# Kernel optimization log

Measured on AMD Instinct MI355X. Metric: run time of the kernel, lower is better.

Reference implementation:

```python
import jax, jax.numpy as jnp
import numpy as np

N_NODES = 100000
N_EDGES = 1600000
F_IN = 128
HID = 128
N_CLS = 40


def setup_inputs() -> dict:
    key = jax.random.key(0)
    ks = jax.random.split(key, 11)
    s = 0.05
    return {
        "X": jax.random.normal(ks[0], (N_NODES, F_IN), dtype=jnp.float32),
        "edge_index": jax.random.randint(ks[1], (2, N_EDGES), 0, N_NODES, dtype=jnp.int64),
        "enc_W": jax.random.normal(ks[2], (HID, F_IN), dtype=jnp.float32) * s,
        "enc_b": jax.random.normal(ks[3], (HID,), dtype=jnp.float32) * s,
        "W1": jax.random.normal(ks[4], (HID, HID), dtype=jnp.float32) * s,
        "b1": jax.random.normal(ks[5], (HID,), dtype=jnp.float32) * s,
        "W2": jax.random.normal(ks[6], (HID, HID), dtype=jnp.float32) * s,
        "b2": jax.random.normal(ks[7], (HID,), dtype=jnp.float32) * s,
        "dec_W": jax.random.normal(ks[8], (N_CLS, HID), dtype=jnp.float32) * s,
        "dec_b": jax.random.normal(ks[9], (N_CLS,), dtype=jnp.float32) * s,
    }


def reference(X, edge_index, enc_W, enc_b, W1, b1, W2, b2, dec_W, dec_b):
    N = X.shape[0]
    # --- add self-loops (PyG GCNConv default) ---
    loop = jnp.arange(N, dtype=edge_index.dtype)
    src = jnp.concatenate([edge_index[0], loop])  # message sources
    dst = jnp.concatenate([edge_index[1], loop])  # aggregation targets
    # --- symmetric normalization: D^{-1/2} A_hat D^{-1/2} ---
    deg = jax.ops.segment_sum(jnp.ones_like(src, dtype=X.dtype), dst, num_segments=N)
    dinv = jnp.where(deg > 0, jax.lax.rsqrt(deg), 0.0)
    norm = dinv[src] * dinv[dst]  # [E+N]

    def gcn_conv(x, W, b):
        h = x @ W.T                               # [N,H] linear transform
        msg = h[src] * norm[:, None]              # gather + scale  [E+N,H]
        agg = jax.ops.segment_sum(msg, dst, num_segments=N)  # scatter-sum
        return agg + b

    x = X @ enc_W.T + enc_b                       # encoder (single Linear)
    x = jax.nn.relu(gcn_conv(x, W1, b1))
    x = jax.nn.relu(gcn_conv(x, W2, b2))
    logits = x @ dec_W.T + dec_b                  # decoder (single Linear)
    return jax.nn.log_softmax(logits, axis=1)
```

## Files before the change

kernel.cpp:

```cpp
#include <hip/hip_runtime.h>
#include <hip/hip_bf16.h>
#include <cstdint>

typedef __bf16 bf16x8 __attribute__((ext_vector_type(8)));
typedef float  f32x4  __attribute__((ext_vector_type(4)));


__global__ __launch_bounds__(256) void bucket_hist_kernel(const int* __restrict__ dst,
                                                          int* __restrict__ bhist,
                                                          int E, int NBK, int shift) {
    __shared__ int lh[1024];
    int t = threadIdx.x;
    for (int i = t; i < 1024; i += 256) lh[i] = 0;
    __syncthreads();
#pragma unroll
    for (int v = 0; v < 4; ++v) {
        int idx = blockIdx.x * 4096 + (v * 256 + t) * 4;
        if (idx + 3 < E) {
            int4 d = *reinterpret_cast<const int4*>(&dst[idx]);
            atomicAdd(&lh[d.x >> shift], 1);
            atomicAdd(&lh[d.y >> shift], 1);
            atomicAdd(&lh[d.z >> shift], 1);
            atomicAdd(&lh[d.w >> shift], 1);
        } else {
            for (int k = 0; k < 4; ++k)
                if (idx + k < E) atomicAdd(&lh[dst[idx + k] >> shift], 1);
        }
    }
    __syncthreads();
    for (int i = t; i < NBK; i += 256)
        if (lh[i]) atomicAdd(&bhist[i], lh[i]);
}

__global__ __launch_bounds__(256) void bucket_scan_kernel(const int* __restrict__ bhist,
                                                          int* __restrict__ bbase,
                                                          int* __restrict__ bcur,
                                                          int NBK, int* __restrict__ offsetsN, int E) {
    int t = threadIdx.x;
    int v0[4]; int s = 0;
#pragma unroll
    for (int k = 0; k < 4; ++k) { int i = t * 4 + k; v0[k] = (i < NBK) ? bhist[i] : 0; s += v0[k]; }
    int lane = t & 63, w = t >> 6;
    int v = s;
#pragma unroll
    for (int o = 1; o < 64; o <<= 1) { int u = __shfl_up(v, o); if (lane >= o) v += u; }
    __shared__ int ws[4];
    if (lane == 63) ws[w] = v;
    __syncthreads();
    if (t == 0) { int r = 0; for (int i = 0; i < 4; ++i) { int x = ws[i]; ws[i] = r; r += x; } }
    __syncthreads();
    int run = ws[w] + (v - s);
#pragma unroll
    for (int k = 0; k < 4; ++k) {
        int i = t * 4 + k;
        if (i < NBK) { bbase[i] = run; bcur[i] = run; run += v0[k]; }
    }
    if (t == 255) bbase[NBK] = E;
    if (t == 0)   *offsetsN = E;
}

__global__ __launch_bounds__(256) void bin_edges_kernel(const int* __restrict__ src,
                                                        const int* __restrict__ dst,
                                                        int* __restrict__ bcur,
                                                        unsigned* __restrict__ binned,
                                                        int E, int NBK, int shift) {
    __shared__ int lh[1024];
    int t = threadIdx.x;
    int mask = (1 << shift) - 1;
    for (int i = t; i < 1024; i += 256) lh[i] = 0;
    __syncthreads();
    int sv[32], dv[32], rk[32];
#pragma unroll
    for (int v = 0; v < 8; ++v) {
        int idx = blockIdx.x * 8192 + (v * 256 + t) * 4;
        if (idx + 3 < E) {
            int4 s4 = *reinterpret_cast<const int4*>(&src[idx]);
            int4 d4 = *reinterpret_cast<const int4*>(&dst[idx]);
            sv[v * 4 + 0] = s4.x; sv[v * 4 + 1] = s4.y; sv[v * 4 + 2] = s4.z; sv[v * 4 + 3] = s4.w;
            dv[v * 4 + 0] = d4.x; dv[v * 4 + 1] = d4.y; dv[v * 4 + 2] = d4.z; dv[v * 4 + 3] = d4.w;
        } else {
            for (int k = 0; k < 4; ++k) {
                sv[v * 4 + k] = (idx + k < E) ? src[idx + k] : 0;
                dv[v * 4 + k] = (idx + k < E) ? dst[idx + k] : -1;
            }
        }
    }
#pragma unroll
    for (int k = 0; k < 32; ++k)
        if (dv[k] >= 0) rk[k] = atomicAdd(&lh[dv[k] >> shift], 1);
    __syncthreads();
    for (int i = t; i < NBK; i += 256) {
        int c = lh[i];
        lh[i] = c ? atomicAdd(&bcur[i], c) : 0;
    }
    __syncthreads();
#pragma unroll
    for (int k = 0; k < 32; ++k) {
        if (dv[k] >= 0) {
            int b = dv[k] >> shift;
            binned[lh[b] + rk[k]] = ((unsigned)sv[k] << shift) | (unsigned)(dv[k] & mask);
        }
    }
}

__global__ __launch_bounds__(256) void bucket_build_kernel(const unsigned* __restrict__ binned,
                                                           const int* __restrict__ bbase,
                                                           int* __restrict__ csr_src,
                                                           int* __restrict__ offsets,
                                                           float* __restrict__ dinv,
                                                           int N, int shift) {
    int b = blockIdx.x;
    int t = threadIdx.x;
    int node0 = b << shift;
    int npb = min(1 << shift, N - node0);
    int bb = bbase[b], be = bbase[b + 1];
    int mask = (1 << shift) - 1;
    __shared__ int ncnt[256], npre[256], ncur[256];
    ncnt[t] = 0;
    __syncthreads();
    for (int e = bb + t; e < be; e += 256) {
        unsigned p = binned[e];
        atomicAdd(&ncnt[p & mask], 1);
    }
    __syncthreads();
    int deg = (t < npb) ? ncnt[t] : 0;
    int v = deg;
    int lane = t & 63, w = t >> 6;
#pragma unroll
    for (int o = 1; o < 64; o <<= 1) { int u = __shfl_up(v, o); if (lane >= o) v += u; }
    __shared__ int ws[4];
    if (lane == 63) ws[w] = v;
    __syncthreads();
    if (t == 0) { int r = 0; for (int i = 0; i < 4; ++i) { int x = ws[i]; ws[i] = r; r += x; } }
    __syncthreads();
    int pre = bb + ws[w] + v - deg;
    npre[t] = pre; ncur[t] = 0;
    __syncthreads();
    for (int e = bb + t; e < be; e += 256) {
        unsigned p = binned[e];
        int l = p & mask;
        int r = atomicAdd(&ncur[l], 1);
        csr_src[npre[l] + r] = (int)(p >> shift);
    }
    if (t < npb) {
        int node = node0 + t;
        offsets[node] = pre;
        dinv[node] = rsqrtf((float)(deg + 1));
    }
}

__global__ __launch_bounds__(128) void prep_weights_kernel(const float* __restrict__ W1,
                                                           const float* __restrict__ encW,
                                                           const float* __restrict__ encb,
                                                           const float* __restrict__ W2,
                                                           const float* __restrict__ decW,
                                                           __hip_bfloat16* __restrict__ Wfb,
                                                           float* __restrict__ bff,
                                                           __hip_bfloat16* __restrict__ W2b,
                                                           __hip_bfloat16* __restrict__ decWb) {
    int i = blockIdx.x;
    int j = threadIdx.x;
    const float* w1r = W1 + (size_t)i * 128;
    float s0 = 0.f, s1 = 0.f, s2 = 0.f, s3 = 0.f;
    for (int k = 0; k < 128; k += 4) {
        s0 += w1r[k + 0] * encW[(size_t)(k + 0) * 128 + j];
        s1 += w1r[k + 1] * encW[(size_t)(k + 1) * 128 + j];
        s2 += w1r[k + 2] * encW[(size_t)(k + 2) * 128 + j];
        s3 += w1r[k + 3] * encW[(size_t)(k + 3) * 128 + j];
    }
    Wfb[(size_t)i * 128 + j] = __float2bfloat16((s0 + s1) + (s2 + s3));
    W2b[(size_t)i * 128 + j] = __float2bfloat16(W2[(size_t)i * 128 + j]);
    if (i < 48) decWb[(size_t)i * 128 + j] = __float2bfloat16(i < 40 ? decW[(size_t)i * 128 + j] : 0.f);
    float t = w1r[j] * encb[j];
#pragma unroll
    for (int o = 32; o; o >>= 1) t += __shfl_down(t, o);
    __shared__ float red[2];
    if ((j & 63) == 0) red[j >> 6] = t;
    __syncthreads();
    if (j == 0) bff[i] = red[0] + red[1];
}

__device__ inline bf16x8 cvt8(float4 lo, float4 hi) {
    union { unsigned short u[8]; bf16x8 v; } t;
    t.u[0] = __builtin_bit_cast(unsigned short, __float2bfloat16(lo.x));
    t.u[1] = __builtin_bit_cast(unsigned short, __float2bfloat16(lo.y));
    t.u[2] = __builtin_bit_cast(unsigned short, __float2bfloat16(lo.z));
    t.u[3] = __builtin_bit_cast(unsigned short, __float2bfloat16(lo.w));
    t.u[4] = __builtin_bit_cast(unsigned short, __float2bfloat16(hi.x));
    t.u[5] = __builtin_bit_cast(unsigned short, __float2bfloat16(hi.y));
    t.u[6] = __builtin_bit_cast(unsigned short, __float2bfloat16(hi.z));
    t.u[7] = __builtin_bit_cast(unsigned short, __float2bfloat16(hi.w));
    return t.v;
}

__global__ __launch_bounds__(256) void gemm_enc_kernel(const float* __restrict__ Ain,
                                                       const __hip_bfloat16* __restrict__ W,
                                                       const float* __restrict__ bias,
                                                       const float* __restrict__ dscale,
                                                       __hip_bfloat16* __restrict__ out, int M) {
    int lane = threadIdx.x & 63;
    int wave = threadIdx.x >> 6;
    int row0 = blockIdx.x * 128 + wave * 32;
    int kgrp = lane >> 4, cl = lane & 15;

    bf16x8 afrag[2][4];
#pragma unroll
    for (int rt = 0; rt < 2; ++rt) {
        int ar = row0 + rt * 16 + cl;
        if (ar >= M) ar = M - 1;
        const float* Ar = Ain + (size_t)ar * 128;
#pragma unroll
        for (int c = 0; c < 4; ++c) {
            const float4* q = reinterpret_cast<const float4*>(Ar + (4 * c + kgrp) * 8);
            afrag[rt][c] = cvt8(q[0], q[1]);
        }
    }

    f32x4 acc[2][8];
#pragma unroll
    for (int rt = 0; rt < 2; ++rt)
#pragma unroll
        for (int t = 0; t < 8; ++t) acc[rt][t] = {0.f, 0.f, 0.f, 0.f};

#pragma unroll
    for (int c = 0; c < 4; ++c) {
#pragma unroll
        for (int t = 0; t < 8; ++t) {
            bf16x8 bfrag = reinterpret_cast<const bf16x8*>(W + (size_t)(t * 16 + cl) * 128)[4 * c + kgrp];
            acc[0][t] = __builtin_amdgcn_mfma_f32_16x16x32_bf16(afrag[0][c], bfrag, acc[0][t], 0, 0, 0);
            acc[1][t] = __builtin_amdgcn_mfma_f32_16x16x32_bf16(afrag[1][c], bfrag, acc[1][t], 0, 0, 0);
        }
    }

#pragma unroll
    for (int rt = 0; rt < 2; ++rt) {
        int rbase = row0 + rt * 16 + kgrp * 4;
#pragma unroll
        for (int i = 0; i < 4; ++i) {
            int r = rbase + i;
            float sc = dscale[(r < M) ? r : (M - 1)];
#pragma unroll
            for (int t = 0; t < 8; ++t) {
                int col = t * 16 + cl;
                float v = (acc[rt][t][i] + bias[col]) * sc;
                unsigned int uv = __builtin_bit_cast(unsigned short, __float2bfloat16(v));
                unsigned int pv = (unsigned int)__shfl_xor((int)uv, 1);
                if (!(lane & 1) && r < M)
                    *reinterpret_cast<unsigned int*>(out + (size_t)r * 128 + col) = (uv & 0xffffu) | (pv << 16);
            }
        }
    }
}

template<int NPW>
__device__ __forceinline__ void agg_phase(const __hip_bfloat16* __restrict__ h,
                                          const int* __restrict__ csr,
                                          const int* __restrict__ offsets,
                                          const float* __restrict__ dinv,
                                          const float* __restrict__ bias,
                                          unsigned* lds, int tile0, int N) {
    int w = threadIdx.x >> 6, lane = threadIdx.x & 63;
    int bc = lane * 2;
    float2 bb = *reinterpret_cast<const float2*>(&bias[bc]);
    int base = tile0 + w * NPW;
    int oidx = base + (lane < NPW ? lane : NPW);
    if (oidx > N) oidx = N;
    int off = offsets[oidx];

    int j0a[NPW], dga[NPW], nda[NPW];
    unsigned qs[NPW];
#pragma unroll
    for (int i = 0; i < NPW; ++i) {
        int node = base + i;
        nda[i] = __builtin_amdgcn_readfirstlane((node < N) ? node : (N - 1));
        j0a[i] = __builtin_amdgcn_readfirstlane(__shfl(off, i));
        int j1 = __builtin_amdgcn_readfirstlane(__shfl(off, i + 1));
        dga[i] = j1 - j0a[i];
        qs[i] = *reinterpret_cast<const unsigned*>(&h[(size_t)nda[i] * 128 + bc]);
    }
    int sc[NPW][8];
#pragma unroll
    for (int i = 0; i < NPW; ++i)
#pragma unroll
        for (int k = 0; k < 8; ++k)
            sc[i][k] = csr[j0a[i] + k];
    unsigned qn[8];
#pragma unroll
    for (int k = 0; k < 8; ++k)
        qn[k] = *reinterpret_cast<const unsigned*>(&h[(size_t)sc[0][k] * 128 + bc]);

#pragma unroll
    for (int i = 0; i < NPW; ++i) {
        int j0 = j0a[i], dg = dga[i];
        int node = base + i;
        bool live = node < N;

        unsigned qc[8];
#pragma unroll
        for (int k = 0; k < 8; ++k) qc[k] = qn[k];
        if (i + 1 < NPW) {
#pragma unroll
            for (int k = 0; k < 8; ++k)
                qn[k] = *reinterpret_cast<const unsigned*>(&h[(size_t)sc[i + 1][k] * 128 + bc]);
        }

        float ax[8], ay[8];
        ax[0] = __builtin_bit_cast(float, qs[i] << 16);
        ay[0] = __builtin_bit_cast(float, qs[i] & 0xffff0000u);
#pragma unroll
        for (int k = 1; k < 8; ++k) { ax[k] = 0.f; ay[k] = 0.f; }

#pragma unroll
        for (int k = 0; k < 8; ++k) {
            unsigned q = (k < dg) ? qc[k] : 0u;
            ax[k] += __builtin_bit_cast(float, q << 16);
            ay[k] += __builtin_bit_cast(float, q & 0xffff0000u);
        }
        int nb = (dg + 7) >> 3;
        for (int b = 1; b < nb; ++b) {
            int jb = j0 + 8 * b;
            int s[8];
#pragma unroll
            for (int k = 0; k < 8; ++k) s[k] = csr[jb + k];
            unsigned q[8];
#pragma unroll
            for (int k = 0; k < 8; ++k)
                q[k] = *reinterpret_cast<const unsigned*>(&h[(size_t)s[k] * 128 + bc]);
            int rem = dg - 8 * b;
#pragma unroll
            for (int k = 0; k < 8; ++k) {
                unsigned qq = (k < rem) ? q[k] : 0u;
                ax[k] += __builtin_bit_cast(float, qq << 16);
                ay[k] += __builtin_bit_cast(float, qq & 0xffff0000u);
            }
        }

        float sx = ((ax[0] + ax[1]) + (ax[2] + ax[3])) + ((ax[4] + ax[5]) + (ax[6] + ax[7]));
        float sy = ((ay[0] + ay[1]) + (ay[2] + ay[3])) + ((ay[4] + ay[5]) + (ay[6] + ay[7]));
        float dd = dinv[nda[i]];
        float ox = fmaxf(dd * sx + bb.x, 0.f);
        float oy = fmaxf(dd * sy + bb.y, 0.f);
        unsigned ow = (unsigned)__builtin_bit_cast(unsigned short, __float2bfloat16(ox)) |
                      ((unsigned)__builtin_bit_cast(unsigned short, __float2bfloat16(oy)) << 16);
        if (!live) ow = 0u;
        int row = w * NPW + i;
        lds[row * 64 + (lane ^ ((row & 15) << 2))] = ow;
    }
}

__global__ __launch_bounds__(512, 8) void agg_gemm_kernel(const __hip_bfloat16* __restrict__ h,
                                                          const int* __restrict__ csr,
                                                          const int* __restrict__ offsets,
                                                          const float* __restrict__ dinv,
                                                          const float* __restrict__ bias,
                                                          const __hip_bfloat16* __restrict__ W,
                                                          __hip_bfloat16* __restrict__ out, int N) {
    __shared__ unsigned lds[32 * 64];
    int tile0 = blockIdx.x * 32;
    agg_phase<4>(h, csr, offsets, dinv, bias, lds, tile0, N);
    __syncthreads();

    int lane = threadIdx.x & 63, w = threadIdx.x >> 6;
    int kgrp = lane >> 4, cl = lane & 15;
    int rt = w & 1, cq = w >> 1;
    bf16x8 afrag[4];
#pragma unroll
    for (int c = 0; c < 4; ++c) {
        int kk = 4 * c + kgrp;
        int row = rt * 16 + cl;
        afrag[c] = *reinterpret_cast<const bf16x8*>(&lds[row * 64 + ((kk * 4) ^ (cl << 2))]);
    }
    f32x4 acc[2];
#pragma unroll
    for (int t = 0; t < 2; ++t) acc[t] = {0.f, 0.f, 0.f, 0.f};
#pragma unroll
    for (int c = 0; c < 4; ++c)
#pragma unroll
        for (int t = 0; t < 2; ++t) {
            bf16x8 bfrag = reinterpret_cast<const bf16x8*>(W + (size_t)(cq * 32 + t * 16 + cl) * 128)[4 * c + kgrp];
            acc[t] = __builtin_amdgcn_mfma_f32_16x16x32_bf16(afrag[c], bfrag, acc[t], 0, 0, 0);
        }
#pragma unroll
    for (int i = 0; i < 4; ++i) {
        int r = tile0 + rt * 16 + kgrp * 4 + i;
        float sc = dinv[(r < N) ? r : (N - 1)];
#pragma unroll
        for (int t = 0; t < 2; ++t) {
            int col = cq * 32 + t * 16 + cl;
            float v = acc[t][i] * sc;
            unsigned uv = __builtin_bit_cast(unsigned short, __float2bfloat16(v));
            unsigned pv = (unsigned)__shfl_xor((int)uv, 1);
            if (!(lane & 1) && r < N)
                *reinterpret_cast<unsigned*>(out + (size_t)r * 128 + col) = (uv & 0xffffu) | (pv << 16);
        }
    }
}

__global__ __launch_bounds__(512, 8) void agg_dec_kernel(const __hip_bfloat16* __restrict__ h,
                                                         const int* __restrict__ csr,
                                                         const int* __restrict__ offsets,
                                                         const float* __restrict__ dinv,
                                                         const float* __restrict__ bias,
                                                         const __hip_bfloat16* __restrict__ Wd,
                                                         const float* __restrict__ bd,
                                                         float* __restrict__ out, int N) {
    __shared__ unsigned lds[32 * 64];
    int tile0 = blockIdx.x * 32;
    agg_phase<4>(h, csr, offsets, dinv, bias, lds, tile0, N);
    __syncthreads();

    int lane = threadIdx.x & 63, w = threadIdx.x >> 6;
    if (w >= 2) return;
    int kgrp = lane >> 4, cl = lane & 15;
    bf16x8 afrag[4];
#pragma unroll
    for (int c = 0; c < 4; ++c) {
        int kk = 4 * c + kgrp;
        int row = w * 16 + cl;
        afrag[c] = *reinterpret_cast<const bf16x8*>(&lds[row * 64 + ((kk * 4) ^ (cl << 2))]);
    }
    f32x4 acc[3];
#pragma unroll
    for (int t = 0; t < 3; ++t) acc[t] = {0.f, 0.f, 0.f, 0.f};
#pragma unroll
    for (int c = 0; c < 4; ++c)
#pragma unroll
        for (int t = 0; t < 3; ++t) {
            bf16x8 bfrag = reinterpret_cast<const bf16x8*>(Wd + (size_t)(t * 16 + cl) * 128)[4 * c + kgrp];
            acc[t] = __builtin_amdgcn_mfma_f32_16x16x32_bf16(afrag[c], bfrag, acc[t], 0, 0, 0);
        }

    float v[3][4];
#pragma unroll
    for (int t = 0; t < 3; ++t) {
        int col = t * 16 + cl;
        float bv = (col < 40) ? bd[col] : 0.f;
#pragma unroll
        for (int i = 0; i < 4; ++i)
            v[t][i] = (col < 40) ? (acc[t][i] + bv) : -INFINITY;
    }
#pragma unroll
    for (int i = 0; i < 4; ++i) {
        float m = fmaxf(fmaxf(v[0][i], v[1][i]), v[2][i]);
#pragma unroll
        for (int o = 1; o < 16; o <<= 1) m = fmaxf(m, __shfl_xor(m, o));
        float s = 0.f;
#pragma unroll
        for (int t = 0; t < 3; ++t) s += (v[t][i] > -INFINITY) ? __expf(v[t][i] - m) : 0.f;
#pragma unroll
        for (int o = 1; o < 16; o <<= 1) s += __shfl_xor(s, o);
        float lse = __logf(s);
        int r = tile0 + w * 16 + kgrp * 4 + i;
        if (r < N) {
#pragma unroll
            for (int t = 0; t < 3; ++t) {
                int col = t * 16 + cl;
                if (col < 40) out[(size_t)r * 40 + col] = v[t][i] - m - lse;
            }
        }
    }
}

extern "C" void kernel_launch(void* const* d_in, const int* in_sizes, int n_in,
                              void* d_out, int out_size, void* d_ws, size_t ws_size,
                              hipStream_t stream) {
    const float* X    = (const float*)d_in[0];
    const int*   ei   = (const int*)d_in[1];
    const float* encW = (const float*)d_in[2];
    const float* encb = (const float*)d_in[3];
    const float* W1   = (const float*)d_in[4];
    const float* b1   = (const float*)d_in[5];
    const float* W2   = (const float*)d_in[6];
    const float* b2   = (const float*)d_in[7];
    const float* decW = (const float*)d_in[8];
    const float* decb = (const float*)d_in[9];

    const int N = in_sizes[0] / 128;
    const int E = in_sizes[1] / 2;
    const int* src = ei;
    const int* dst = ei + E;

    int shift = 7;
    while ((((N - 1) >> shift) + 1) > 1024) ++shift;
    const int NBK = ((N - 1) >> shift) + 1;

    uint8_t* p = (uint8_t*)d_ws;
    auto carve = [&](size_t bytes) -> void* {
        uint8_t* r = p;
        p += (bytes + 255) & ~(size_t)255;
        return (void*)r;
    };
    int*   offsets = (int*)carve((size_t)(N + 1) * 4);
    float* dinv    = (float*)carve((size_t)N * 4);
    int*   bhist   = (int*)carve(1025 * 4);
    int*   bbase   = (int*)carve(1025 * 4);
    int*   bcur    = (int*)carve(1024 * 4);
    int*   csr_src = (int*)carve(((size_t)E + 8) * 4);
    __hip_bfloat16* Wfb   = (__hip_bfloat16*)carve(16384 * 2);
    __hip_bfloat16* W2b   = (__hip_bfloat16*)carve(16384 * 2);
    __hip_bfloat16* decWb = (__hip_bfloat16*)carve(48 * 128 * 2);
    float*          bff   = (float*)carve(128 * 4);
    __hip_bfloat16* xb    = (__hip_bfloat16*)carve((size_t)N * 128 * 2);
    __hip_bfloat16* hb    = (__hip_bfloat16*)carve((size_t)N * 128 * 2);
    unsigned* binned = (unsigned*)xb;

    prep_weights_kernel<<<128, 128, 0, stream>>>(W1, encW, encb, W2, decW, Wfb, bff, W2b, decWb);

    hipMemsetAsync(bhist, 0, (size_t)NBK * 4, stream);
    hipMemsetAsync(csr_src + E, 0, 8 * 4, stream);
    bucket_hist_kernel<<<(E + 4095) / 4096, 256, 0, stream>>>(dst, bhist, E, NBK, shift);
    bucket_scan_kernel<<<1, 256, 0, stream>>>(bhist, bbase, bcur, NBK, &offsets[N], E);
    bin_edges_kernel<<<(E + 8191) / 8192, 256, 0, stream>>>(src, dst, bcur, binned, E, NBK, shift);
    bucket_build_kernel<<<NBK, 256, 0, stream>>>(binned, bbase, csr_src, offsets, dinv, N, shift);

    int gblocks = (N + 127) / 128;
    int tblocks = (N + 31) / 32;
    gemm_enc_kernel<<<gblocks, 256, 0, stream>>>(X, Wfb, bff, dinv, hb, N);
    agg_gemm_kernel<<<tblocks, 512, 0, stream>>>(hb, csr_src, offsets, dinv, b1, W2b, xb, N);
    agg_dec_kernel<<<tblocks, 512, 0, stream>>>(xb, csr_src, offsets, dinv, b2, decWb, decb,
                                                (float*)d_out, N);
}
```

Before: 231.6 us.

## Shrink fused aggregate+GEMM blocks to one wavefront handling four nodes

The fused aggregation+GEMM and aggregation+decoder kernels move from 512-thread blocks covering 32 nodes to 64-thread single-wave blocks covering 4 nodes. The MFMA stage now runs on a 16-row tile where only 4 rows are real, and each wave loops over all output column tiles. This drops the block-wide barrier over 8 waves and the large LDS tile, so the scheduler can overlap waves independently. The cost is a quarter of the MFMA work being useful, more redundant weight loads per node, and more blocks to launch.

```diff
diff --git a/kernel.cpp b/kernel.cpp
--- a/kernel.cpp
+++ b/kernel.cpp
@@ -252,25 +252,23 @@
     }
 }
 
-template<int NPW>
-__device__ __forceinline__ void agg_phase(const __hip_bfloat16* __restrict__ h,
-                                          const int* __restrict__ csr,
-                                          const int* __restrict__ offsets,
-                                          const float* __restrict__ dinv,
-                                          const float* __restrict__ bias,
-                                          unsigned* lds, int tile0, int N) {
-    int w = threadIdx.x >> 6, lane = threadIdx.x & 63;
+__device__ __forceinline__ void agg_phase4(const __hip_bfloat16* __restrict__ h,
+                                           const int* __restrict__ csr,
+                                           const int* __restrict__ offsets,
+                                           const float* __restrict__ dinv,
+                                           const float* __restrict__ bias,
+                                           unsigned* lds, int base, int N) {
+    int lane = threadIdx.x & 63;
     int bc = lane * 2;
     float2 bb = *reinterpret_cast<const float2*>(&bias[bc]);
-    int base = tile0 + w * NPW;
-    int oidx = base + (lane < NPW ? lane : NPW);
+    int oidx = base + (lane < 4 ? lane : 4);
     if (oidx > N) oidx = N;
     int off = offsets[oidx];
 
-    int j0a[NPW], dga[NPW], nda[NPW];
-    unsigned qs[NPW];
-#pragma unroll
-    for (int i = 0; i < NPW; ++i) {
+    int j0a[4], dga[4], nda[4];
+    unsigned qs[4];
+#pragma unroll
+    for (int i = 0; i < 4; ++i) {
         int node = base + i;
         nda[i] = __builtin_amdgcn_readfirstlane((node < N) ? node : (N - 1));
         j0a[i] = __builtin_amdgcn_readfirstlane(__shfl(off, i));
@@ -278,9 +276,9 @@
         dga[i] = j1 - j0a[i];
         qs[i] = *reinterpret_cast<const unsigned*>(&h[(size_t)nda[i] * 128 + bc]);
     }
-    int sc[NPW][8];
-#pragma unroll
-    for (int i = 0; i < NPW; ++i)
+    int sc[4][8];
+#pragma unroll
+    for (int i = 0; i < 4; ++i)
 #pragma unroll
         for (int k = 0; k < 8; ++k)
             sc[i][k] = csr[j0a[i] + k];
@@ -290,15 +288,14 @@
         qn[k] = *reinterpret_cast<const unsigned*>(&h[(size_t)sc[0][k] * 128 + bc]);
 
 #pragma unroll
-    for (int i = 0; i < NPW; ++i) {
+    for (int i = 0; i < 4; ++i) {
         int j0 = j0a[i], dg = dga[i];
-        int node = base + i;
-        bool live = node < N;
+        bool live = (base + i) < N;
 
         unsigned qc[8];
 #pragma unroll
         for (int k = 0; k < 8; ++k) qc[k] = qn[k];
-        if (i + 1 < NPW) {
+        if (i + 1 < 4) {
 #pragma unroll
             for (int k = 0; k < 8; ++k)
                 qn[k] = *reinterpret_cast<const unsigned*>(&h[(size_t)sc[i + 1][k] * 128 + bc]);
@@ -343,81 +340,76 @@
         unsigned ow = (unsigned)__builtin_bit_cast(unsigned short, __float2bfloat16(ox)) |
                       ((unsigned)__builtin_bit_cast(unsigned short, __float2bfloat16(oy)) << 16);
         if (!live) ow = 0u;
-        int row = w * NPW + i;
-        lds[row * 64 + (lane ^ ((row & 15) << 2))] = ow;
-    }
-}
-
-__global__ __launch_bounds__(512, 8) void agg_gemm_kernel(const __hip_bfloat16* __restrict__ h,
-                                                          const int* __restrict__ csr,
-                                                          const int* __restrict__ offsets,
-                                                          const float* __restrict__ dinv,
-                                                          const float* __restrict__ bias,
-                                                          const __hip_bfloat16* __restrict__ W,
-                                                          __hip_bfloat16* __restrict__ out, int N) {
-    __shared__ unsigned lds[32 * 64];
-    int tile0 = blockIdx.x * 32;
-    agg_phase<4>(h, csr, offsets, dinv, bias, lds, tile0, N);
-    __syncthreads();
-
-    int lane = threadIdx.x & 63, w = threadIdx.x >> 6;
-    int kgrp = lane >> 4, cl = lane & 15;
-    int rt = w & 1, cq = w >> 1;
-    bf16x8 afrag[4];
-#pragma unroll
-    for (int c = 0; c < 4; ++c) {
-        int kk = 4 * c + kgrp;
-        int row = rt * 16 + cl;
-        afrag[c] = *reinterpret_cast<const bf16x8*>(&lds[row * 64 + ((kk * 4) ^ (cl << 2))]);
-    }
-    f32x4 acc[2];
-#pragma unroll
-    for (int t = 0; t < 2; ++t) acc[t] = {0.f, 0.f, 0.f, 0.f};
-#pragma unroll
-    for (int c = 0; c < 4; ++c)
-#pragma unroll
-        for (int t = 0; t < 2; ++t) {
-            bf16x8 bfrag = reinterpret_cast<const bf16x8*>(W + (size_t)(cq * 32 + t * 16 + cl) * 128)[4 * c + kgrp];
-            acc[t] = __builtin_amdgcn_mfma_f32_16x16x32_bf16(afrag[c], bfrag, acc[t], 0, 0, 0);
-        }
-#pragma unroll
-    for (int i = 0; i < 4; ++i) {
-        int r = tile0 + rt * 16 + kgrp * 4 + i;
-        float sc = dinv[(r < N) ? r : (N - 1)];
-#pragma unroll
-        for (int t = 0; t < 2; ++t) {
-            int col = cq * 32 + t * 16 + cl;
-            float v = acc[t][i] * sc;
-            unsigned uv = __builtin_bit_cast(unsigned short, __float2bfloat16(v));
-            unsigned pv = (unsigned)__shfl_xor((int)uv, 1);
-            if (!(lane & 1) && r < N)
-                *reinterpret_cast<unsigned*>(out + (size_t)r * 128 + col) = (uv & 0xffffu) | (pv << 16);
-        }
-    }
-}
-
-__global__ __launch_bounds__(512, 8) void agg_dec_kernel(const __hip_bfloat16* __restrict__ h,
+        lds[i * 64 + (lane ^ (i << 2))] = ow;
+    }
+}
+
+__global__ __launch_bounds__(64, 8) void agg_gemm_kernel(const __hip_bfloat16* __restrict__ h,
                                                          const int* __restrict__ csr,
                                                          const int* __restrict__ offsets,
                                                          const float* __restrict__ dinv,
                                                          const float* __restrict__ bias,
-                                                         const __hip_bfloat16* __restrict__ Wd,
-                                                         const float* __restrict__ bd,
-                                                         float* __restrict__ out, int N) {
-    __shared__ unsigned lds[32 * 64];
-    int tile0 = blockIdx.x * 32;
-    agg_phase<4>(h, csr, offsets, dinv, bias, lds, tile0, N);
-    __syncthreads();
-
-    int lane = threadIdx.x & 63, w = threadIdx.x >> 6;
-    if (w >= 2) return;
+                                                         const __hip_bfloat16* __restrict__ W,
+                                                         __hip_bfloat16* __restrict__ out, int N) {
+    __shared__ unsigned lds[4 * 64];
+    int base = blockIdx.x * 4;
+    agg_phase4(h, csr, offsets, dinv, bias, lds, base, N);
+    __syncthreads();
+
+    int lane = threadIdx.x & 63;
     int kgrp = lane >> 4, cl = lane & 15;
+    int row = cl & 3;
     bf16x8 afrag[4];
 #pragma unroll
     for (int c = 0; c < 4; ++c) {
         int kk = 4 * c + kgrp;
-        int row = w * 16 + cl;
-        afrag[c] = *reinterpret_cast<const bf16x8*>(&lds[row * 64 + ((kk * 4) ^ (cl << 2))]);
+        afrag[c] = *reinterpret_cast<const bf16x8*>(&lds[row * 64 + ((kk * 4) ^ (row << 2))]);
+    }
+    float sc4[4];
+#pragma unroll
+    for (int i = 0; i < 4; ++i) sc4[i] = dinv[min(base + i, N - 1)];
+
+#pragma unroll
+    for (int t = 0; t < 8; ++t) {
+        f32x4 acc = {0.f, 0.f, 0.f, 0.f};
+#pragma unroll
+        for (int c = 0; c < 4; ++c) {
+            bf16x8 bfrag = reinterpret_cast<const bf16x8*>(W + (size_t)(t * 16 + cl) * 128)[4 * c + kgrp];
+            acc = __builtin_amdgcn_mfma_f32_16x16x32_bf16(afrag[c], bfrag, acc, 0, 0, 0);
+        }
+#pragma unroll
+        for (int i = 0; i < 4; ++i) {
+            float v = acc[i] * sc4[i];
+            unsigned uv = __builtin_bit_cast(unsigned short, __float2bfloat16(v));
+            unsigned pv = (unsigned)__shfl_xor((int)uv, 1);
+            if (!(lane & 1) && lane < 16 && base + i < N)
+                *reinterpret_cast<unsigned*>(out + (size_t)(base + i) * 128 + t * 16 + cl) =
+                    (uv & 0xffffu) | (pv << 16);
+        }
+    }
+}
+
+__global__ __launch_bounds__(64, 8) void agg_dec_kernel(const __hip_bfloat16* __restrict__ h,
+                                                        const int* __restrict__ csr,
+                                                        const int* __restrict__ offsets,
+                                                        const float* __restrict__ dinv,
+                                                        const float* __restrict__ bias,
+                                                        const __hip_bfloat16* __restrict__ Wd,
+                                                        const float* __restrict__ bd,
+                                                        float* __restrict__ out, int N) {
+    __shared__ unsigned lds[4 * 64];
+    int base = blockIdx.x * 4;
+    agg_phase4(h, csr, offsets, dinv, bias, lds, base, N);
+    __syncthreads();
+
+    int lane = threadIdx.x & 63;
+    int kgrp = lane >> 4, cl = lane & 15;
+    int row = cl & 3;
+    bf16x8 afrag[4];
+#pragma unroll
+    for (int c = 0; c < 4; ++c) {
+        int kk = 4 * c + kgrp;
+        afrag[c] = *reinterpret_cast<const bf16x8*>(&lds[row * 64 + ((kk * 4) ^ (row << 2))]);
     }
     f32x4 acc[3];
 #pragma unroll
@@ -450,8 +442,8 @@
 #pragma unroll
         for (int o = 1; o < 16; o <<= 1) s += __shfl_xor(s, o);
         float lse = __logf(s);
-        int r = tile0 + w * 16 + kgrp * 4 + i;
-        if (r < N) {
+        int r = base + i;
+        if (lane < 16 && r < N) {
 #pragma unroll
             for (int t = 0; t < 3; ++t) {
                 int col = t * 16 + cl;
@@ -495,7 +487,7 @@
     int*   bhist   = (int*)carve(1025 * 4);
     int*   bbase   = (int*)carve(1025 * 4);
     int*   bcur    = (int*)carve(1024 * 4);
-    int*   csr_src = (int*)carve(((size_t)E + 8) * 4);
+    int*   csr_src = (int*)carve(((size_t)E + 16) * 4);
     __hip_bfloat16* Wfb   = (__hip_bfloat16*)carve(16384 * 2);
     __hip_bfloat16* W2b   = (__hip_bfloat16*)carve(16384 * 2);
     __hip_bfloat16* decWb = (__hip_bfloat16*)carve(48 * 128 * 2);
@@ -507,16 +499,16 @@
     prep_weights_kernel<<<128, 128, 0, stream>>>(W1, encW, encb, W2, decW, Wfb, bff, W2b, decWb);
 
     hipMemsetAsync(bhist, 0, (size_t)NBK * 4, stream);
-    hipMemsetAsync(csr_src + E, 0, 8 * 4, stream);
+    hipMemsetAsync(csr_src + E, 0, 16 * 4, stream);
     bucket_hist_kernel<<<(E + 4095) / 4096, 256, 0, stream>>>(dst, bhist, E, NBK, shift);
     bucket_scan_kernel<<<1, 256, 0, stream>>>(bhist, bbase, bcur, NBK, &offsets[N], E);
     bin_edges_kernel<<<(E + 8191) / 8192, 256, 0, stream>>>(src, dst, bcur, binned, E, NBK, shift);
     bucket_build_kernel<<<NBK, 256, 0, stream>>>(binned, bbase, csr_src, offsets, dinv, N, shift);
 
     int gblocks = (N + 127) / 128;
-    int tblocks = (N + 31) / 32;
+    int tblocks = (N + 3) / 4;
     gemm_enc_kernel<<<gblocks, 256, 0, stream>>>(X, Wfb, bff, dinv, hb, N);
-    agg_gemm_kernel<<<tblocks, 512, 0, stream>>>(hb, csr_src, offsets, dinv, b1, W2b, xb, N);
-    agg_dec_kernel<<<tblocks, 512, 0, stream>>>(xb, csr_src, offsets, dinv, b2, decWb, decb,
-                                                (float*)d_out, N);
-}
+    agg_gemm_kernel<<<tblocks, 64, 0, stream>>>(hb, csr_src, offsets, dinv, b1, W2b, xb, N);
+    agg_dec_kernel<<<tblocks, 64, 0, stream>>>(xb, csr_src, offsets, dinv, b2, decWb, decb,
+                                               (float*)d_out, N);
+}
```

After: 279.2 us. 20.5% more time.
